# Optimization experiments

Measured on AMD Instinct MI355X. Metric: run time of the kernel, lower is better.

## Reference

```python
import math
import jax, jax.numpy as jnp
import numpy as np


def setup_inputs() -> dict:
    key0 = jax.random.key(0)
    ks = jax.random.split(key0, 6)
    BS_NH, NK, DK = 32, 256, 64
    return {
        "query": jax.random.normal(ks[0], (BS_NH, NK, DK), dtype=jnp.float32),
        "key": jax.random.normal(ks[1], (BS_NH, NK, DK), dtype=jnp.float32),
        "value": jax.random.normal(ks[2], (BS_NH, NK, DK), dtype=jnp.float32),
        "sa": jax.random.normal(ks[3], (BS_NH, NK, NK, DK), dtype=jnp.float32),
        "sv": jax.random.normal(ks[4], (BS_NH, NK, NK, DK), dtype=jnp.float32),
        "mask": jax.random.randint(ks[5], (BS_NH, NK, NK), 0, 2, dtype=jnp.int32),
    }


def reference(query, key, value, sa, sv, mask):
    bs_nh, nk, dk = query.shape
    # scores: (bs_nh, nk, nk)
    scores = jnp.einsum("bqd,bkd->bqk", query, key) / math.sqrt(dk)
    scores = jnp.where(mask == 0, jnp.float32(-1e9), scores)
    attention = jax.nn.softmax(scores, axis=-1)
    v_val = jnp.einsum("bqk,bkd->bqd", attention, value)  # (bs_nh, nk, dk)
    sa_r = sa.reshape(-1, nk, nk, dk)
    sv_r = sv.reshape(-1, nk, nk, dk)
    s_val = (sa_r * sv_r).mean(axis=2)  # (bs_nh, nk, dk)
    out = jnp.concatenate([v_val, s_val], axis=-1)  # (bs_nh, nk, 2*dk)
    return out, attention
```

## Files before the change

### kernel.cpp

```cpp
#include <hip/hip_runtime.h>

constexpr int BSNH = 32;
constexpr int NK   = 256;
constexpr int DK   = 64;
constexpr int ROWS = 4;
constexpr int RS4  = NK * (DK / 4);

typedef float f32x4 __attribute__((ext_vector_type(4)));

__device__ __forceinline__ float4 shfl_down4(float4 v, int off) {
    float4 r;
    r.x = __shfl_down(v.x, off, 64);
    r.y = __shfl_down(v.y, off, 64);
    r.z = __shfl_down(v.z, off, 64);
    r.w = __shfl_down(v.w, off, 64);
    return r;
}

__device__ __forceinline__ void add4(float4& a, const float4 b) {
    a.x += b.x; a.y += b.y; a.z += b.z; a.w += b.w;
}

__global__ __launch_bounds__(256) void sdpa_split_kernel(
    const float* __restrict__ Q, const float* __restrict__ K,
    const float* __restrict__ V, const float* __restrict__ SA,
    const float* __restrict__ SV, const int* __restrict__ MASK,
    float* __restrict__ OUT,
    float* __restrict__ ATTN)
{
    const int role = blockIdx.x & 1;
    const int p    = blockIdx.x >> 1;
    const int b    = p >> 6;
    const int q0   = (p & 63) * ROWS;
    const int tid  = threadIdx.x;
    const int lane = tid & 63;
    const int wave = tid >> 6;
    const int d4   = tid & 15;
    const int kt   = tid >> 4;

    __shared__ float  qs[ROWS][DK];
    __shared__ float  attn_s[ROWS][NK];
    __shared__ float4 red4[4][ROWS][16];

    if (role == 0) {
        const f32x4* sa4 = reinterpret_cast<const f32x4*>(SA) + (size_t)(b * NK + q0) * RS4;
        const f32x4* sv4 = reinterpret_cast<const f32x4*>(SV) + (size_t)(b * NK + q0) * RS4;
        f32x4 acc[ROWS];
        #pragma unroll
        for (int r = 0; r < ROWS; ++r) acc[r] = (f32x4)(0.f);
        #pragma unroll 2
        for (int kk = 0; kk < 16; ++kk) {
            const size_t o = (size_t)(kt + kk * 16) * 16 + d4;
            f32x4 av[ROWS], bv[ROWS];
            #pragma unroll
            for (int r = 0; r < ROWS; ++r) {
                av[r] = __builtin_nontemporal_load(&sa4[(size_t)r * RS4 + o]);
                bv[r] = __builtin_nontemporal_load(&sv4[(size_t)r * RS4 + o]);
            }
            #pragma unroll
            for (int r = 0; r < ROWS; ++r)
                acc[r] += av[r] * bv[r];
        }
        float4 accf[ROWS];
        #pragma unroll
        for (int r = 0; r < ROWS; ++r) {
            accf[r] = make_float4(acc[r].x, acc[r].y, acc[r].z, acc[r].w);
            add4(accf[r], shfl_down4(accf[r], 32));
            add4(accf[r], shfl_down4(accf[r], 16));
        }
        if (lane < 16) {
            #pragma unroll
            for (int r = 0; r < ROWS; ++r) red4[wave][r][lane] = accf[r];
        }
        __syncthreads();
        if (tid < 64) {
            const int r = tid >> 4, c = tid & 15;
            float4 res = red4[0][r][c];
            add4(res, red4[1][r][c]);
            add4(res, red4[2][r][c]);
            add4(res, red4[3][r][c]);
            const float scale = 1.f / 256.f;
            res.x *= scale; res.y *= scale; res.z *= scale; res.w *= scale;
            reinterpret_cast<float4*>(OUT)[(size_t)(b * NK + q0 + r) * 32 + 16 + c] = res;
        }
        return;
    }


    qs[wave][lane] = Q[((size_t)(b * NK + q0)) * DK + tid];
    __syncthreads();

    {
        const float4* krow = reinterpret_cast<const float4*>(K + ((size_t)b * NK + tid) * DK);
        float sc0 = 0.f, sc1 = 0.f, sc2 = 0.f, sc3 = 0.f;
        #pragma unroll
        for (int i = 0; i < DK / 4; ++i) {
            const float4 kv = krow[i];
            sc0 = fmaf(qs[0][4*i+0], kv.x, sc0); sc0 = fmaf(qs[0][4*i+1], kv.y, sc0);
            sc0 = fmaf(qs[0][4*i+2], kv.z, sc0); sc0 = fmaf(qs[0][4*i+3], kv.w, sc0);
            sc1 = fmaf(qs[1][4*i+0], kv.x, sc1); sc1 = fmaf(qs[1][4*i+1], kv.y, sc1);
            sc1 = fmaf(qs[1][4*i+2], kv.z, sc1); sc1 = fmaf(qs[1][4*i+3], kv.w, sc1);
            sc2 = fmaf(qs[2][4*i+0], kv.x, sc2); sc2 = fmaf(qs[2][4*i+1], kv.y, sc2);
            sc2 = fmaf(qs[2][4*i+2], kv.z, sc2); sc2 = fmaf(qs[2][4*i+3], kv.w, sc2);
            sc3 = fmaf(qs[3][4*i+0], kv.x, sc3); sc3 = fmaf(qs[3][4*i+1], kv.y, sc3);
            sc3 = fmaf(qs[3][4*i+2], kv.z, sc3); sc3 = fmaf(qs[3][4*i+3], kv.w, sc3);
        }
        const int* mrow = MASK + ((size_t)(b * NK + q0)) * NK + tid;
        const int m0 = __builtin_nontemporal_load(&mrow[0 * NK]);
        const int m1 = __builtin_nontemporal_load(&mrow[1 * NK]);
        const int m2 = __builtin_nontemporal_load(&mrow[2 * NK]);
        const int m3 = __builtin_nontemporal_load(&mrow[3 * NK]);
        attn_s[0][tid] = (m0 == 0) ? -1e9f : sc0 * 0.125f;
        attn_s[1][tid] = (m1 == 0) ? -1e9f : sc1 * 0.125f;
        attn_s[2][tid] = (m2 == 0) ? -1e9f : sc2 * 0.125f;
        attn_s[3][tid] = (m3 == 0) ? -1e9f : sc3 * 0.125f;
    }
    __syncthreads();

    {
        const int r = wave;
        float v0 = attn_s[r][lane];
        float v1 = attn_s[r][lane + 64];
        float v2 = attn_s[r][lane + 128];
        float v3 = attn_s[r][lane + 192];
        float m = fmaxf(fmaxf(v0, v1), fmaxf(v2, v3));
        #pragma unroll
        for (int off = 32; off >= 1; off >>= 1)
            m = fmaxf(m, __shfl_xor(m, off, 64));
        const float e0 = __expf(v0 - m), e1 = __expf(v1 - m),
                    e2 = __expf(v2 - m), e3 = __expf(v3 - m);
        float s = e0 + e1 + e2 + e3;
        #pragma unroll
        for (int off = 32; off >= 1; off >>= 1)
            s += __shfl_xor(s, off, 64);
        const float inv = 1.0f / s;
        const float a0 = e0 * inv, a1 = e1 * inv, a2 = e2 * inv, a3 = e3 * inv;
        attn_s[r][lane]       = a0;
        attn_s[r][lane + 64]  = a1;
        attn_s[r][lane + 128] = a2;
        attn_s[r][lane + 192] = a3;
        float* arow = ATTN + ((size_t)(b * NK + q0 + r)) * NK;
        arow[lane]       = a0;
        arow[lane + 64]  = a1;
        arow[lane + 128] = a2;
        arow[lane + 192] = a3;
    }
    __syncthreads();

    {
        const float4* v4 = reinterpret_cast<const float4*>(V + (size_t)b * NK * DK);
        float4 acc[ROWS];
        #pragma unroll
        for (int r = 0; r < ROWS; ++r) acc[r] = make_float4(0.f, 0.f, 0.f, 0.f);
        #pragma unroll 4
        for (int kk = 0; kk < 16; ++kk) {
            const int kidx = kt + kk * 16;
            const float4 vv = v4[kidx * 16 + d4];
            #pragma unroll
            for (int r = 0; r < ROWS; ++r) {
                const float w = attn_s[r][kidx];
                acc[r].x = fmaf(w, vv.x, acc[r].x);
                acc[r].y = fmaf(w, vv.y, acc[r].y);
                acc[r].z = fmaf(w, vv.z, acc[r].z);
                acc[r].w = fmaf(w, vv.w, acc[r].w);
            }
        }
        #pragma unroll
        for (int r = 0; r < ROWS; ++r) {
            add4(acc[r], shfl_down4(acc[r], 32));
            add4(acc[r], shfl_down4(acc[r], 16));
        }
        if (lane < 16) {
            #pragma unroll
            for (int r = 0; r < ROWS; ++r) red4[wave][r][lane] = acc[r];
        }
        __syncthreads();
        if (tid < 64) {
            const int r = tid >> 4, c = tid & 15;
            float4 res = red4[0][r][c];
            add4(res, red4[1][r][c]);
            add4(res, red4[2][r][c]);
            add4(res, red4[3][r][c]);
            reinterpret_cast<float4*>(OUT)[(size_t)(b * NK + q0 + r) * 32 + c] = res;
        }
    }
}

extern "C" void kernel_launch(void* const* d_in, const int* in_sizes, int n_in,
                              void* d_out, int out_size, void* d_ws, size_t ws_size,
                              hipStream_t stream) {
    const float* Q    = (const float*)d_in[0];
    const float* K    = (const float*)d_in[1];
    const float* V    = (const float*)d_in[2];
    const float* SA   = (const float*)d_in[3];
    const float* SV   = (const float*)d_in[4];
    const int*   MASK = (const int*)d_in[5];

    float* OUT  = (float*)d_out;
    float* ATTN = OUT + (size_t)BSNH * NK * (2 * DK);

    sdpa_split_kernel<<<dim3(2 * BSNH * NK / ROWS), dim3(256), 0, stream>>>(
        Q, K, V, SA, SV, MASK, OUT, ATTN);
}
```

Before: 216.5 us.

## Merge stream and attention roles into one block with staggered phase order

Each block now runs both the sa*sv mean reduction and the attention computation for its four query rows, instead of launching separate blocks per role. Groups of eight blocks alternate which phase runs first, so memory-bound streaming overlaps with compute-heavier attention across concurrently resident blocks. Output and attention stores become nontemporal. The grid is halved and each block runs longer, which can reduce the parallelism available to saturate HBM bandwidth.

```diff
diff --git a/kernel.cpp b/kernel.cpp
--- a/kernel.cpp
+++ b/kernel.cpp
@@ -21,17 +21,16 @@
     a.x += b.x; a.y += b.y; a.z += b.z; a.w += b.w;
 }
 
-__global__ __launch_bounds__(256) void sdpa_split_kernel(
+__global__ __launch_bounds__(256) void sdpa_stagger_kernel(
     const float* __restrict__ Q, const float* __restrict__ K,
     const float* __restrict__ V, const float* __restrict__ SA,
     const float* __restrict__ SV, const int* __restrict__ MASK,
     float* __restrict__ OUT,
     float* __restrict__ ATTN)
 {
-    const int role = blockIdx.x & 1;
-    const int p    = blockIdx.x >> 1;
-    const int b    = p >> 6;
-    const int q0   = (p & 63) * ROWS;
+    const int blk  = blockIdx.x;
+    const int b    = blk >> 6;
+    const int q0   = (blk & 63) * ROWS;
     const int tid  = threadIdx.x;
     const int lane = tid & 63;
     const int wave = tid >> 6;
@@ -42,7 +41,7 @@
     __shared__ float  attn_s[ROWS][NK];
     __shared__ float4 red4[4][ROWS][16];
 
-    if (role == 0) {
+    auto stream_phase = [&]() {
         const f32x4* sa4 = reinterpret_cast<const f32x4*>(SA) + (size_t)(b * NK + q0) * RS4;
         const f32x4* sv4 = reinterpret_cast<const f32x4*>(SV) + (size_t)(b * NK + q0) * RS4;
         f32x4 acc[ROWS];
@@ -80,109 +79,125 @@
             add4(res, red4[2][r][c]);
             add4(res, red4[3][r][c]);
             const float scale = 1.f / 256.f;
-            res.x *= scale; res.y *= scale; res.z *= scale; res.w *= scale;
-            reinterpret_cast<float4*>(OUT)[(size_t)(b * NK + q0 + r) * 32 + 16 + c] = res;
-        }
-        return;
-    }
-
-
-    qs[wave][lane] = Q[((size_t)(b * NK + q0)) * DK + tid];
-    __syncthreads();
-
-    {
-        const float4* krow = reinterpret_cast<const float4*>(K + ((size_t)b * NK + tid) * DK);
-        float sc0 = 0.f, sc1 = 0.f, sc2 = 0.f, sc3 = 0.f;
-        #pragma unroll
-        for (int i = 0; i < DK / 4; ++i) {
-            const float4 kv = krow[i];
-            sc0 = fmaf(qs[0][4*i+0], kv.x, sc0); sc0 = fmaf(qs[0][4*i+1], kv.y, sc0);
-            sc0 = fmaf(qs[0][4*i+2], kv.z, sc0); sc0 = fmaf(qs[0][4*i+3], kv.w, sc0);
-            sc1 = fmaf(qs[1][4*i+0], kv.x, sc1); sc1 = fmaf(qs[1][4*i+1], kv.y, sc1);
-            sc1 = fmaf(qs[1][4*i+2], kv.z, sc1); sc1 = fmaf(qs[1][4*i+3], kv.w, sc1);
-            sc2 = fmaf(qs[2][4*i+0], kv.x, sc2); sc2 = fmaf(qs[2][4*i+1], kv.y, sc2);
-            sc2 = fmaf(qs[2][4*i+2], kv.z, sc2); sc2 = fmaf(qs[2][4*i+3], kv.w, sc2);
-            sc3 = fmaf(qs[3][4*i+0], kv.x, sc3); sc3 = fmaf(qs[3][4*i+1], kv.y, sc3);
-            sc3 = fmaf(qs[3][4*i+2], kv.z, sc3); sc3 = fmaf(qs[3][4*i+3], kv.w, sc3);
-        }
-        const int* mrow = MASK + ((size_t)(b * NK + q0)) * NK + tid;
-        const int m0 = __builtin_nontemporal_load(&mrow[0 * NK]);
-        const int m1 = __builtin_nontemporal_load(&mrow[1 * NK]);
-        const int m2 = __builtin_nontemporal_load(&mrow[2 * NK]);
-        const int m3 = __builtin_nontemporal_load(&mrow[3 * NK]);
-        attn_s[0][tid] = (m0 == 0) ? -1e9f : sc0 * 0.125f;
-        attn_s[1][tid] = (m1 == 0) ? -1e9f : sc1 * 0.125f;
-        attn_s[2][tid] = (m2 == 0) ? -1e9f : sc2 * 0.125f;
-        attn_s[3][tid] = (m3 == 0) ? -1e9f : sc3 * 0.125f;
-    }
-    __syncthreads();
-
-    {
-        const int r = wave;
-        float v0 = attn_s[r][lane];
-        float v1 = attn_s[r][lane + 64];
-        float v2 = attn_s[r][lane + 128];
-        float v3 = attn_s[r][lane + 192];
-        float m = fmaxf(fmaxf(v0, v1), fmaxf(v2, v3));
-        #pragma unroll
-        for (int off = 32; off >= 1; off >>= 1)
-            m = fmaxf(m, __shfl_xor(m, off, 64));
-        const float e0 = __expf(v0 - m), e1 = __expf(v1 - m),
-                    e2 = __expf(v2 - m), e3 = __expf(v3 - m);
-        float s = e0 + e1 + e2 + e3;
-        #pragma unroll
-        for (int off = 32; off >= 1; off >>= 1)
-            s += __shfl_xor(s, off, 64);
-        const float inv = 1.0f / s;
-        const float a0 = e0 * inv, a1 = e1 * inv, a2 = e2 * inv, a3 = e3 * inv;
-        attn_s[r][lane]       = a0;
-        attn_s[r][lane + 64]  = a1;
-        attn_s[r][lane + 128] = a2;
-        attn_s[r][lane + 192] = a3;
-        float* arow = ATTN + ((size_t)(b * NK + q0 + r)) * NK;
-        arow[lane]       = a0;
-        arow[lane + 64]  = a1;
-        arow[lane + 128] = a2;
-        arow[lane + 192] = a3;
-    }
-    __syncthreads();
-
-    {
-        const float4* v4 = reinterpret_cast<const float4*>(V + (size_t)b * NK * DK);
-        float4 acc[ROWS];
-        #pragma unroll
-        for (int r = 0; r < ROWS; ++r) acc[r] = make_float4(0.f, 0.f, 0.f, 0.f);
-        #pragma unroll 4
-        for (int kk = 0; kk < 16; ++kk) {
-            const int kidx = kt + kk * 16;
-            const float4 vv = v4[kidx * 16 + d4];
+            f32x4 t;
+            t.x = res.x * scale; t.y = res.y * scale;
+            t.z = res.z * scale; t.w = res.w * scale;
+            __builtin_nontemporal_store(
+                t, &reinterpret_cast<f32x4*>(OUT)[(size_t)(b * NK + q0 + r) * 32 + 16 + c]);
+        }
+    };
+
+    auto attn_phase = [&]() {
+        qs[wave][lane] = Q[((size_t)(b * NK + q0)) * DK + tid];
+        __syncthreads();
+
+        {
+            const float4* krow = reinterpret_cast<const float4*>(K + ((size_t)b * NK + tid) * DK);
+            float sc0 = 0.f, sc1 = 0.f, sc2 = 0.f, sc3 = 0.f;
+            #pragma unroll
+            for (int i = 0; i < DK / 4; ++i) {
+                const float4 kv = krow[i];
+                sc0 = fmaf(qs[0][4*i+0], kv.x, sc0); sc0 = fmaf(qs[0][4*i+1], kv.y, sc0);
+                sc0 = fmaf(qs[0][4*i+2], kv.z, sc0); sc0 = fmaf(qs[0][4*i+3], kv.w, sc0);
+                sc1 = fmaf(qs[1][4*i+0], kv.x, sc1); sc1 = fmaf(qs[1][4*i+1], kv.y, sc1);
+                sc1 = fmaf(qs[1][4*i+2], kv.z, sc1); sc1 = fmaf(qs[1][4*i+3], kv.w, sc1);
+                sc2 = fmaf(qs[2][4*i+0], kv.x, sc2); sc2 = fmaf(qs[2][4*i+1], kv.y, sc2);
+                sc2 = fmaf(qs[2][4*i+2], kv.z, sc2); sc2 = fmaf(qs[2][4*i+3], kv.w, sc2);
+                sc3 = fmaf(qs[3][4*i+0], kv.x, sc3); sc3 = fmaf(qs[3][4*i+1], kv.y, sc3);
+                sc3 = fmaf(qs[3][4*i+2], kv.z, sc3); sc3 = fmaf(qs[3][4*i+3], kv.w, sc3);
+            }
+            const int* mrow = MASK + ((size_t)(b * NK + q0)) * NK + tid;
+            const int m0 = __builtin_nontemporal_load(&mrow[0 * NK]);
+            const int m1 = __builtin_nontemporal_load(&mrow[1 * NK]);
+            const int m2 = __builtin_nontemporal_load(&mrow[2 * NK]);
+            const int m3 = __builtin_nontemporal_load(&mrow[3 * NK]);
+            attn_s[0][tid] = (m0 == 0) ? -1e9f : sc0 * 0.125f;
+            attn_s[1][tid] = (m1 == 0) ? -1e9f : sc1 * 0.125f;
+            attn_s[2][tid] = (m2 == 0) ? -1e9f : sc2 * 0.125f;
+            attn_s[3][tid] = (m3 == 0) ? -1e9f : sc3 * 0.125f;
+        }
+        __syncthreads();
+
+        {
+            const int r = wave;
+            float v0 = attn_s[r][lane];
+            float v1 = attn_s[r][lane + 64];
+            float v2 = attn_s[r][lane + 128];
+            float v3 = attn_s[r][lane + 192];
+            float m = fmaxf(fmaxf(v0, v1), fmaxf(v2, v3));
+            #pragma unroll
+            for (int off = 32; off >= 1; off >>= 1)
+                m = fmaxf(m, __shfl_xor(m, off, 64));
+            const float e0 = __expf(v0 - m), e1 = __expf(v1 - m),
+                        e2 = __expf(v2 - m), e3 = __expf(v3 - m);
+            float s = e0 + e1 + e2 + e3;
+            #pragma unroll
+            for (int off = 32; off >= 1; off >>= 1)
+                s += __shfl_xor(s, off, 64);
+            const float inv = 1.0f / s;
+            const float a0 = e0 * inv, a1 = e1 * inv, a2 = e2 * inv, a3 = e3 * inv;
+            attn_s[r][lane]       = a0;
+            attn_s[r][lane + 64]  = a1;
+            attn_s[r][lane + 128] = a2;
+            attn_s[r][lane + 192] = a3;
+            float* arow = ATTN + ((size_t)(b * NK + q0 + r)) * NK;
+            __builtin_nontemporal_store(a0, &arow[lane]);
+            __builtin_nontemporal_store(a1, &arow[lane + 64]);
+            __builtin_nontemporal_store(a2, &arow[lane + 128]);
+            __builtin_nontemporal_store(a3, &arow[lane + 192]);
+        }
+        __syncthreads();
+
+        {
+            const float4* v4 = reinterpret_cast<const float4*>(V + (size_t)b * NK * DK);
+            float4 acc[ROWS];
+            #pragma unroll
+            for (int r = 0; r < ROWS; ++r) acc[r] = make_float4(0.f, 0.f, 0.f, 0.f);
+            #pragma unroll 4
+            for (int kk = 0; kk < 16; ++kk) {
+                const int kidx = kt + kk * 16;
+                const float4 vv = v4[kidx * 16 + d4];
+                #pragma unroll
+                for (int r = 0; r < ROWS; ++r) {
+                    const float w = attn_s[r][kidx];
+                    acc[r].x = fmaf(w, vv.x, acc[r].x);
+                    acc[r].y = fmaf(w, vv.y, acc[r].y);
+                    acc[r].z = fmaf(w, vv.z, acc[r].z);
+                    acc[r].w = fmaf(w, vv.w, acc[r].w);
+                }
+            }
             #pragma unroll
             for (int r = 0; r < ROWS; ++r) {
-                const float w = attn_s[r][kidx];
-                acc[r].x = fmaf(w, vv.x, acc[r].x);
-                acc[r].y = fmaf(w, vv.y, acc[r].y);
-                acc[r].z = fmaf(w, vv.z, acc[r].z);
-                acc[r].w = fmaf(w, vv.w, acc[r].w);
-            }
-        }
-        #pragma unroll
-        for (int r = 0; r < ROWS; ++r) {
-            add4(acc[r], shfl_down4(acc[r], 32));
-            add4(acc[r], shfl_down4(acc[r], 16));
-        }
-        if (lane < 16) {
-            #pragma unroll
-            for (int r = 0; r < ROWS; ++r) red4[wave][r][lane] = acc[r];
-        }
-        __syncthreads();
-        if (tid < 64) {
-            const int r = tid >> 4, c = tid & 15;
-            float4 res = red4[0][r][c];
-            add4(res, red4[1][r][c]);
-            add4(res, red4[2][r][c]);
-            add4(res, red4[3][r][c]);
-            reinterpret_cast<float4*>(OUT)[(size_t)(b * NK + q0 + r) * 32 + c] = res;
-        }
+                add4(acc[r], shfl_down4(acc[r], 32));
+                add4(acc[r], shfl_down4(acc[r], 16));
+            }
+            if (lane < 16) {
+                #pragma unroll
+                for (int r = 0; r < ROWS; ++r) red4[wave][r][lane] = acc[r];
+            }
+            __syncthreads();
+            if (tid < 64) {
+                const int r = tid >> 4, c = tid & 15;
+                float4 res = red4[0][r][c];
+                add4(res, red4[1][r][c]);
+                add4(res, red4[2][r][c]);
+                add4(res, red4[3][r][c]);
+                f32x4 t;
+                t.x = res.x; t.y = res.y; t.z = res.z; t.w = res.w;
+                __builtin_nontemporal_store(
+                    t, &reinterpret_cast<f32x4*>(OUT)[(size_t)(b * NK + q0 + r) * 32 + c]);
+            }
+        }
+    };
+
+    if (((blk >> 3) & 1) == 0) {
+        attn_phase();
+        __syncthreads();
+        stream_phase();
+    } else {
+        stream_phase();
+        __syncthreads();
+        attn_phase();
     }
 }
 
@@ -199,6 +214,6 @@
     float* OUT  = (float*)d_out;
     float* ATTN = OUT + (size_t)BSNH * NK * (2 * DK);
 
-    sdpa_split_kernel<<<dim3(2 * BSNH * NK / ROWS), dim3(256), 0, stream>>>(
+    sdpa_stagger_kernel<<<dim3(BSNH * NK / ROWS), dim3(256), 0, stream>>>(
         Q, K, V, SA, SV, MASK, OUT, ATTN);
 }
```

Result: faster. 194.2 us (-10.3%).
